# Kernel tuning notes

Measured on AMD Instinct MI355X. Metric: run time of the kernel, lower is better.

The kernel has to match this reference:

```python
import jax, jax.numpy as jnp
import numpy as np

B, S, D = 4, 4096, 1024
STATE = 1024
HID = 4 * D
EPS_NORM = 1e-6           # RMSNorm module eps
EPS_FP32 = 1.1920929e-7   # torch F.rms_norm default eps = finfo(fp32).eps


def rms_norm(x, eps):
    # no learned weight (RMSNorm(dim=-1) has weight=None)
    return x * jax.lax.rsqrt(jnp.mean(jnp.square(x), axis=-1, keepdims=True) + eps)


def setup_inputs() -> dict:
    key = jax.random.key(0)
    ks = jax.random.split(key, 8)
    scale_d = 1.0 / np.sqrt(D)
    scale_s = 1.0 / np.sqrt(STATE)
    scale_h = 1.0 / np.sqrt(HID)
    return {
        "x": jax.random.normal(ks[0], (B, S, D), jnp.float32),
        "x0": jax.random.normal(ks[1], (B, S, D), jnp.float32),
        "Wu": jax.random.normal(ks[2], (STATE, D), jnp.float32) * scale_d,
        "Wg": jax.random.normal(ks[3], (STATE, D), jnp.float32) * scale_d,
        "Wo": jax.random.normal(ks[4], (D, STATE), jnp.float32) * scale_s,
        "Wfc": jax.random.normal(ks[5], (HID, D), jnp.float32) * scale_d,
        "Wproj": jax.random.normal(ks[6], (D, HID), jnp.float32) * scale_h,
        "memory_mix": jnp.ones((D,), jnp.float32),
        "mlp_scale": jnp.ones((D,), jnp.float32),
        "resid_mix": jnp.stack([jnp.ones((D,), jnp.float32), jnp.zeros((D,), jnp.float32)]),
    }


def reference(x, x0, Wu, Wg, Wo, Wfc, Wproj, memory_mix, mlp_scale, resid_mix):
    # residual mix of x and x0
    x = resid_mix[0][None, None, :] * x + resid_mix[1][None, None, :] * x0

    # --- CausalPrefixMemory branch ---
    h = rms_norm(x, EPS_NORM)
    update = jnp.einsum('bsd,kd->bsk', h, Wu)
    gate = jax.nn.sigmoid(jnp.einsum('bsd,kd->bsk', h, Wg))
    memory = jnp.cumsum(gate * update, axis=1)          # [B,S,STATE]
    denom = jnp.arange(1, S + 1, dtype=jnp.float32)[None, :, None]
    m = rms_norm(memory / denom, EPS_FP32)
    mem_out = jnp.einsum('bsk,dk->bsd', m, Wo)
    x = x + memory_mix[None, None, :] * mem_out

    # --- MLP branch: relu^2 ---
    h2 = rms_norm(x, EPS_NORM)
    r = jax.nn.relu(jnp.einsum('bsd,hd->bsh', h2, Wfc))
    mlp_out = jnp.einsum('bsh,dh->bsd', jnp.square(r), Wproj)
    x = x + mlp_scale[None, None, :] * mlp_out
    return x
```

## Files before the change

kernel.cpp:

```cpp
#include <hip/hip_runtime.h>
#include <stdint.h>

typedef unsigned short u16;
typedef __attribute__((ext_vector_type(8))) short s16x8;
typedef __attribute__((ext_vector_type(4))) float f32x4;

__device__ __forceinline__ u16 f2bf(float f) {
  uint32_t u = __float_as_uint(f);
  uint32_t r = (u + 0x7FFFu + ((u >> 16) & 1u)) >> 16;
  return (u16)r;
}

__device__ __forceinline__ void gll16(const void* g, void* lds) {
  __builtin_amdgcn_global_load_lds(
      (const __attribute__((address_space(1))) uint32_t*)g,
      (__attribute__((address_space(3))) uint32_t*)lds, 16, 0, 0);
}

__device__ __forceinline__ void xcd_swz(int& bx, int& by) {
  int gx = gridDim.x;
  int lin = blockIdx.y * gx + blockIdx.x;
  int cpx = (gx * gridDim.y) >> 3;
  int nl = (lin & 7) * cpx + (lin >> 3);
  bx = nl % gx;
  by = nl / gx;
}

__global__ __launch_bounds__(256) void k_f2b(const float* __restrict__ src,
                                             u16* __restrict__ dst, int n) {
  int i = (blockIdx.x * 256 + threadIdx.x) * 4;
  if (i < n) {
    float4 v = *(const float4*)(src + i);
    ushort4 o;
    o.x = f2bf(v.x); o.y = f2bf(v.y); o.z = f2bf(v.z); o.w = f2bf(v.w);
    *(ushort4*)(dst + i) = o;
  }
}

template <bool MIX>
__global__ __launch_bounds__(256) void k_rms(const float* __restrict__ X,
                                             const float* __restrict__ X0,
                                             const float* __restrict__ rmix,
                                             float* __restrict__ XMout,
                                             u16* __restrict__ Hout, float eps) {
  const int row = blockIdx.x, t = threadIdx.x;
  const size_t base = (size_t)row * 1024;
  float4 v;
  if (MIX) {
    float4 a = ((const float4*)(X + base))[t];
    float4 b = ((const float4*)(X0 + base))[t];
    float4 c0 = ((const float4*)rmix)[t];
    float4 c1 = ((const float4*)(rmix + 1024))[t];
    v.x = c0.x * a.x + c1.x * b.x;
    v.y = c0.y * a.y + c1.y * b.y;
    v.z = c0.z * a.z + c1.z * b.z;
    v.w = c0.w * a.w + c1.w * b.w;
  } else {
    v = ((const float4*)(X + base))[t];
  }
  float ss = v.x * v.x + v.y * v.y + v.z * v.z + v.w * v.w;
#pragma unroll
  for (int o = 32; o > 0; o >>= 1) ss += __shfl_xor(ss, o);
  __shared__ float red[4];
  if ((t & 63) == 0) red[t >> 6] = ss;
  __syncthreads();
  float tot = red[0] + red[1] + red[2] + red[3];
  float sc = rsqrtf(tot * (1.0f / 1024.0f) + eps);
  if (MIX) ((float4*)(XMout + base))[t] = v;
  ushort4 hv;
  hv.x = f2bf(v.x * sc); hv.y = f2bf(v.y * sc);
  hv.z = f2bf(v.z * sc); hv.w = f2bf(v.w * sc);
  ((ushort4*)(Hout + base))[t] = hv;
}

__global__ __launch_bounds__(256) void k_scan1(const float* __restrict__ P,
                                               float* __restrict__ CS) {
  int blk = blockIdx.x;
  int chunk = blk & 255, b = blk >> 8;
  const float4* p = (const float4*)(P + ((size_t)b * 4096 + chunk * 16) * 1024)
                    + threadIdx.x;
  float4 s = {0.f, 0.f, 0.f, 0.f};
#pragma unroll
  for (int i = 0; i < 16; ++i) {
    float4 v = p[(size_t)i * 256];
    s.x += v.x; s.y += v.y; s.z += v.z; s.w += v.w;
  }
  ((float4*)(CS + ((size_t)b * 256 + chunk) * 1024))[threadIdx.x] = s;
}

__global__ __launch_bounds__(256) void k_scan2(float* __restrict__ CS) {
  int idx = blockIdx.x * 256 + threadIdx.x;
  int b = idx >> 10, k = idx & 1023;
  float run = 0.f;
  for (int c = 0; c < 256; ++c) {
    size_t o = ((size_t)b * 256 + c) * 1024 + k;
    float v = CS[o];
    CS[o] = run;
    run += v;
  }
}

__global__ __launch_bounds__(64) void k_scan3f(const float* __restrict__ P,
                                               const float* __restrict__ CS,
                                               u16* __restrict__ Mout) {
  int blk = blockIdx.x;
  int chunk = blk & 255, b = blk >> 8;
  const int t = threadIdx.x;
  const float4* cs4 = (const float4*)(CS + ((size_t)b * 256 + chunk) * 1024);
  float4 run[4];
#pragma unroll
  for (int q = 0; q < 4; ++q) run[q] = cs4[q * 64 + t];
  const float4* p4 = (const float4*)(P + ((size_t)b * 4096 + chunk * 16) * 1024);
  u16* mo = Mout + ((size_t)b * 4096 + chunk * 16) * 1024;
  const int rowbase = chunk * 16;
#pragma unroll 2
  for (int i = 0; i < 16; ++i) {
    float4 v[4];
#pragma unroll
    for (int q = 0; q < 4; ++q) v[q] = p4[(size_t)i * 256 + q * 64 + t];
    const float inv = 1.0f / (float)(rowbase + i + 1);
    float4 y[4];
    float ss = 0.f;
#pragma unroll
    for (int q = 0; q < 4; ++q) {
      run[q].x += v[q].x; run[q].y += v[q].y;
      run[q].z += v[q].z; run[q].w += v[q].w;
      y[q].x = run[q].x * inv; y[q].y = run[q].y * inv;
      y[q].z = run[q].z * inv; y[q].w = run[q].w * inv;
      ss += y[q].x * y[q].x + y[q].y * y[q].y
          + y[q].z * y[q].z + y[q].w * y[q].w;
    }
#pragma unroll
    for (int o = 32; o > 0; o >>= 1) ss += __shfl_xor(ss, o);
    float sc = rsqrtf(ss * (1.0f / 1024.0f) + 1.1920929e-7f);
#pragma unroll
    for (int q = 0; q < 4; ++q) {
      ushort4 hv;
      hv.x = f2bf(y[q].x * sc); hv.y = f2bf(y[q].y * sc);
      hv.z = f2bf(y[q].z * sc); hv.w = f2bf(y[q].w * sc);
      *(ushort4*)(mo + (size_t)i * 1024 + (q * 64 + t) * 4) = hv;
    }
  }
}

__global__ __launch_bounds__(256, 2) void gemm_dual(
    const u16* __restrict__ A, const u16* __restrict__ Bu,
    const u16* __restrict__ Bg, float* __restrict__ P, int K) {
  __shared__ __align__(16) u16 As[128 * 64];
  __shared__ __align__(16) u16 Us[64 * 64];
  __shared__ __align__(16) u16 Gs[64 * 64];
  const int t = threadIdx.x;
  const int lane = t & 63, wid = t >> 6;
  int bx, by;
  xcd_swz(bx, by);
  const int m0 = by * 128, n0 = bx * 64;
  const int wm = wid * 32;
  const int l15 = lane & 15, lhi = lane >> 4;

  size_t gA[4], gU[2];
#pragma unroll
  for (int i = 0; i < 4; ++i) {
    int j = i * 256 + t;
    int row = j >> 3;
    int k16 = (j & 7) ^ (row & 7);
    gA[i] = (size_t)(m0 + row) * K + k16 * 8;
  }
#pragma unroll
  for (int i = 0; i < 2; ++i) {
    int j = i * 256 + t;
    int row = j >> 3;
    int k16 = (j & 7) ^ (row & 7);
    gU[i] = (size_t)(n0 + row) * K + k16 * 8;
  }

  f32x4 au[2][4], ag[2][4];
#pragma unroll
  for (int mi = 0; mi < 2; ++mi)
#pragma unroll
    for (int ni = 0; ni < 4; ++ni) { au[mi][ni] = 0.0f; ag[mi][ni] = 0.0f; }

  for (int kb = 0; kb < K; kb += 64) {
#pragma unroll
    for (int i = 0; i < 4; ++i) {
      int j = i * 256 + t;
      gll16(A + gA[i] + kb, &As[j * 8]);
    }
#pragma unroll
    for (int i = 0; i < 2; ++i) {
      int j = i * 256 + t;
      gll16(Bu + gU[i] + kb, &Us[j * 8]);
      gll16(Bg + gU[i] + kb, &Gs[j * 8]);
    }
    __syncthreads();
#pragma unroll
    for (int kc = 0; kc < 2; ++kc) {
      s16x8 af[2], uf[4], gf[4];
#pragma unroll
      for (int mi = 0; mi < 2; ++mi) {
        int row = wm + mi * 16 + l15;
        int k16 = (kc * 4 + lhi) ^ (row & 7);
        af[mi] = *(const s16x8*)&As[row * 64 + k16 * 8];
      }
#pragma unroll
      for (int ni = 0; ni < 4; ++ni) {
        int row = ni * 16 + l15;
        int k16 = (kc * 4 + lhi) ^ (row & 7);
        uf[ni] = *(const s16x8*)&Us[row * 64 + k16 * 8];
        gf[ni] = *(const s16x8*)&Gs[row * 64 + k16 * 8];
      }
#pragma unroll
      for (int mi = 0; mi < 2; ++mi)
#pragma unroll
        for (int ni = 0; ni < 4; ++ni) {
          au[mi][ni] = __builtin_amdgcn_mfma_f32_16x16x32_bf16(
              af[mi], uf[ni], au[mi][ni], 0, 0, 0);
          ag[mi][ni] = __builtin_amdgcn_mfma_f32_16x16x32_bf16(
              af[mi], gf[ni], ag[mi][ni], 0, 0, 0);
        }
    }
    __syncthreads();
  }

#pragma unroll
  for (int mi = 0; mi < 2; ++mi) {
    int r0 = m0 + wm + mi * 16 + lhi * 4;
#pragma unroll
    for (int ni = 0; ni < 4; ++ni) {
      int c = n0 + ni * 16 + l15;
#pragma unroll
      for (int j = 0; j < 4; ++j) {
        float u = au[mi][ni][j], g = ag[mi][ni][j];
        P[(size_t)(r0 + j) * 1024 + c] = u / (1.0f + __expf(-g));
      }
    }
  }
}

template <int EPI>
__global__ __launch_bounds__(256, 2) void gemm_bf16(
    const u16* __restrict__ A, const u16* __restrict__ Bw, void* __restrict__ Cout,
    const float* __restrict__ Cadd, const float* __restrict__ colscale,
    int K, int lda, int ldb, int ldc) {
  __shared__ __align__(16) u16 As[128 * 64];
  __shared__ __align__(16) u16 Bs[128 * 64];
  const int t = threadIdx.x;
  const int lane = t & 63, wid = t >> 6;
  int bx, by;
  xcd_swz(bx, by);
  const int m0 = by * 128, n0 = bx * 128;
  const int wm = (wid >> 1) * 64, wn = (wid & 1) * 64;
  const int l15 = lane & 15, lhi = lane >> 4;

  size_t gA[4], gB[4];
#pragma unroll
  for (int i = 0; i < 4; ++i) {
    int j = i * 256 + t;
    int row = j >> 3;
    int k16 = (j & 7) ^ (row & 7);
    gA[i] = (size_t)(m0 + row) * lda + k16 * 8;
    gB[i] = (size_t)(n0 + row) * ldb + k16 * 8;
  }

  f32x4 acc[4][4];
#pragma unroll
  for (int mi = 0; mi < 4; ++mi)
#pragma unroll
    for (int ni = 0; ni < 4; ++ni) acc[mi][ni] = 0.0f;

  for (int kb = 0; kb < K; kb += 64) {
#pragma unroll
    for (int i = 0; i < 4; ++i) {
      int j = i * 256 + t;
      gll16(A + gA[i] + kb, &As[j * 8]);
      gll16(Bw + gB[i] + kb, &Bs[j * 8]);
    }
    __syncthreads();
#pragma unroll
    for (int kc = 0; kc < 2; ++kc) {
      s16x8 af[4], bfr[4];
#pragma unroll
      for (int mi = 0; mi < 4; ++mi) {
        int row = wm + mi * 16 + l15;
        int k16 = (kc * 4 + lhi) ^ (row & 7);
        af[mi] = *(const s16x8*)&As[row * 64 + k16 * 8];
      }
#pragma unroll
      for (int ni = 0; ni < 4; ++ni) {
        int row = wn + ni * 16 + l15;
        int k16 = (kc * 4 + lhi) ^ (row & 7);
        bfr[ni] = *(const s16x8*)&Bs[row * 64 + k16 * 8];
      }
#pragma unroll
      for (int mi = 0; mi < 4; ++mi)
#pragma unroll
        for (int ni = 0; ni < 4; ++ni)
          acc[mi][ni] = __builtin_amdgcn_mfma_f32_16x16x32_bf16(
              af[mi], bfr[ni], acc[mi][ni], 0, 0, 0);
    }
    __syncthreads();
  }

#pragma unroll
  for (int mi = 0; mi < 4; ++mi) {
    int r0 = m0 + wm + mi * 16 + lhi * 4;
#pragma unroll
    for (int ni = 0; ni < 4; ++ni) {
      int c = n0 + wn + ni * 16 + l15;
      float cs = (EPI == 1) ? colscale[c] : 0.f;
#pragma unroll
      for (int j = 0; j < 4; ++j) {
        size_t idx = (size_t)(r0 + j) * ldc + c;
        float v = acc[mi][ni][j];
        if (EPI == 1) {
          ((float*)Cout)[idx] = Cadd[idx] + cs * v;
        } else {
          float rv = fmaxf(v, 0.f);
          ((u16*)Cout)[idx] = f2bf(rv * rv);
        }
      }
    }
  }
}

extern "C" void kernel_launch(void* const* d_in, const int* in_sizes, int n_in,
                              void* d_out, int out_size, void* d_ws, size_t ws_size,
                              hipStream_t stream) {
  const float* x = (const float*)d_in[0];
  const float* x0 = (const float*)d_in[1];
  const float* Wu = (const float*)d_in[2];
  const float* Wg = (const float*)d_in[3];
  const float* Wo = (const float*)d_in[4];
  const float* Wfc = (const float*)d_in[5];
  const float* Wpj = (const float*)d_in[6];
  const float* mmix = (const float*)d_in[7];
  const float* mscale = (const float*)d_in[8];
  const float* rmix = (const float*)d_in[9];
  float* out = (float*)d_out;

  const int M = 16384;
  const size_t MiB = 1024 * 1024;

  char* ws = (char*)d_ws;
  u16* WuB = (u16*)ws;   ws += 2 * MiB;
  u16* WgB = (u16*)ws;   ws += 2 * MiB;
  u16* WoB = (u16*)ws;   ws += 2 * MiB;
  u16* WfcB = (u16*)ws;  ws += 8 * MiB;
  u16* WpjB = (u16*)ws;  ws += 8 * MiB;
  u16* h = (u16*)ws;     ws += 32 * MiB;
  char* pool = ws;
  float* P = (float*)pool;
  float* CS = (float*)(pool + 64 * MiB);
  u16* mB = (u16*)(pool + 68 * MiB);
  u16* R2 = (u16*)pool;
  float* xm = out;

  const bool fullR2 = ws_size >= 182 * MiB;

  k_f2b<<<1024, 256, 0, stream>>>(Wu, WuB, 1024 * 1024);
  k_f2b<<<1024, 256, 0, stream>>>(Wg, WgB, 1024 * 1024);
  k_f2b<<<1024, 256, 0, stream>>>(Wo, WoB, 1024 * 1024);
  k_f2b<<<4096, 256, 0, stream>>>(Wfc, WfcB, 4096 * 1024);
  k_f2b<<<4096, 256, 0, stream>>>(Wpj, WpjB, 4096 * 1024);

  k_rms<true><<<M, 256, 0, stream>>>(x, x0, rmix, xm, h, 1e-6f);

  gemm_dual<<<dim3(16, 128), 256, 0, stream>>>(h, WuB, WgB, P, 1024);

  k_scan1<<<1024, 256, 0, stream>>>(P, CS);
  k_scan2<<<16, 256, 0, stream>>>(CS);
  k_scan3f<<<1024, 64, 0, stream>>>(P, CS, mB);

  gemm_bf16<1><<<dim3(8, 128), 256, 0, stream>>>(mB, WoB, xm, xm, mmix,
                                                 1024, 1024, 1024, 1024);
  k_rms<false><<<M, 256, 0, stream>>>(xm, nullptr, nullptr, nullptr, h, 1e-6f);

  if (fullR2) {
    gemm_bf16<2><<<dim3(32, 128), 256, 0, stream>>>(
        h, WfcB, R2, nullptr, nullptr, 1024, 1024, 1024, 4096);
    gemm_bf16<1><<<dim3(8, 128), 256, 0, stream>>>(
        R2, WpjB, out, out, mscale, 4096, 4096, 4096, 1024);
  } else {
    for (int c = 0; c < 2; ++c) {
      gemm_bf16<2><<<dim3(16, 128), 256, 0, stream>>>(
          h, WfcB + (size_t)c * 2048 * 1024, R2, nullptr, nullptr,
          1024, 1024, 1024, 2048);
      gemm_bf16<1><<<dim3(8, 128), 256, 0, stream>>>(
          R2, WpjB + (size_t)c * 2048, out, out, mscale,
          2048, 2048, 4096, 1024);
    }
  }
}
```

Measured before the change: 520.3 us.

## Replace 128x128 GEMM with 256x256 eight-wave double-buffered pipelined kernel

Replaces the simple single-buffered 128x128 bf16 GEMM with a 256x256-tile, 512-thread kernel. It double-buffers LDS and interleaves next-tile global_load_lds issues with MFMA phases, using explicit barriers, waitcnt and setprio. The aim is to hide global-load latency and raise arithmetic intensity per block for the Wo, Wfc and Wproj GEMMs. The cost is 128KB of LDS and one block per CU, which gives fewer blocks and possible wave-quantization at the smaller grid sizes. Hand-tuned vmcnt counts also raise correctness risk.

Result: slower. 548.1 us (+5.3%).

```diff
diff --git a/kernel.cpp b/kernel.cpp
--- a/kernel.cpp
+++ b/kernel.cpp
@@ -236,76 +236,137 @@
   }
 }
 
+#define SA8(SQ, HF, KB)                                                      \
+  { _Pragma("unroll") for (int c = 0; c < 2; ++c)                            \
+      gll16(A + aoff[c] + (size_t)(HF) * 128 * lda + (KB),                   \
+            (u16*)As + ((SQ) * 2 + (HF)) * 8192 + lo[c]); }
+#define SB8(SQ, HF, KB)                                                      \
+  { _Pragma("unroll") for (int c = 0; c < 2; ++c)                            \
+      gll16(Bw + boff[c] + (size_t)(HF) * 128 * ldb + (KB),                  \
+            (u16*)Bs + ((SQ) * 2 + (HF)) * 8192 + lo[c]); }
+
+#define PH8(PAR, KC, MH, CHK0, STGSTMT, VMSTMT)                              \
+  {                                                                          \
+    if (CHK0) {                                                              \
+      STGSTMT;                                                               \
+      VMSTMT;                                                                \
+      __builtin_amdgcn_s_barrier();                                          \
+      __builtin_amdgcn_sched_barrier(0);                                     \
+    }                                                                        \
+    s16x8 af[4];                                                             \
+    _Pragma("unroll") for (int j = 0; j < 4; ++j) {                          \
+      int row = ((MH) * 4 + j) * 16 + l15;                                   \
+      int cph = (((KC) * 4 + lhi) ^ (row & 7));                              \
+      af[j] = *(const s16x8*)((const u16*)As + ((PAR) * 2 + wr) * 8192       \
+                              + row * 64 + cph * 8);                         \
+    }                                                                        \
+    if ((MH) == 0) {                                                         \
+      _Pragma("unroll") for (int ni = 0; ni < 4; ++ni) {                     \
+        int row = rb + ni * 16 + l15;                                        \
+        int cph = (((KC) * 4 + lhi) ^ (row & 7));                            \
+        bf[ni] = *(const s16x8*)((const u16*)Bs + ((PAR) * 2 + hb) * 8192    \
+                                 + row * 64 + cph * 8);                      \
+      }                                                                      \
+    }                                                                        \
+    if (!(CHK0)) {                                                           \
+      STGSTMT;                                                               \
+      __builtin_amdgcn_s_barrier();                                          \
+    }                                                                        \
+    asm volatile("s_waitcnt lgkmcnt(0)" ::: "memory");                       \
+    __builtin_amdgcn_sched_barrier(0);                                       \
+    __builtin_amdgcn_s_setprio(1);                                           \
+    _Pragma("unroll") for (int j = 0; j < 4; ++j)                            \
+      _Pragma("unroll") for (int ni = 0; ni < 4; ++ni)                       \
+        acc[(MH) * 4 + j][ni] = __builtin_amdgcn_mfma_f32_16x16x32_bf16(     \
+            af[j], bf[ni], acc[(MH) * 4 + j][ni], 0, 0, 0);                  \
+    __builtin_amdgcn_s_setprio(0);                                           \
+    __builtin_amdgcn_s_barrier();                                            \
+    __builtin_amdgcn_sched_barrier(0);                                       \
+  }
+
 template <int EPI>
-__global__ __launch_bounds__(256, 2) void gemm_bf16(
-    const u16* __restrict__ A, const u16* __restrict__ Bw, void* __restrict__ Cout,
-    const float* __restrict__ Cadd, const float* __restrict__ colscale,
-    int K, int lda, int ldb, int ldc) {
-  __shared__ __align__(16) u16 As[128 * 64];
-  __shared__ __align__(16) u16 Bs[128 * 64];
+__global__ __launch_bounds__(512, 1) void gemm8p(
+    const u16* __restrict__ A, const u16* __restrict__ Bw,
+    void* __restrict__ Cout, const float* __restrict__ Cadd,
+    const float* __restrict__ colscale, int K, int lda, int ldb, int ldc) {
+  __shared__ __align__(16) u16 As[2][2][128][64];
+  __shared__ __align__(16) u16 Bs[2][2][128][64];
   const int t = threadIdx.x;
   const int lane = t & 63, wid = t >> 6;
   int bx, by;
   xcd_swz(bx, by);
-  const int m0 = by * 128, n0 = bx * 128;
-  const int wm = (wid >> 1) * 64, wn = (wid & 1) * 64;
+  const int m0 = by * 256, n0 = bx * 256;
+  const int wr = wid >> 2, wc = wid & 3;
   const int l15 = lane & 15, lhi = lane >> 4;
-
-  size_t gA[4], gB[4];
-#pragma unroll
-  for (int i = 0; i < 4; ++i) {
-    int j = i * 256 + t;
-    int row = j >> 3;
-    int k16 = (j & 7) ^ (row & 7);
-    gA[i] = (size_t)(m0 + row) * lda + k16 * 8;
-    gB[i] = (size_t)(n0 + row) * ldb + k16 * 8;
-  }
-
-  f32x4 acc[4][4];
-#pragma unroll
-  for (int mi = 0; mi < 4; ++mi)
+  const int hb = wc >> 1;
+  const int rb = (wc & 1) * 64;
+
+  uint32_t aoff[2], boff[2];
+  int lo[2];
+#pragma unroll
+  for (int c = 0; c < 2; ++c) {
+    int j = c * 512 + t;
+    int row = j >> 3, p8 = j & 7;
+    int lg = p8 ^ (row & 7);
+    aoff[c] = (uint32_t)(m0 + row) * lda + lg * 8;
+    boff[c] = (uint32_t)(n0 + row) * ldb + lg * 8;
+    lo[c] = j * 8;
+  }
+
+  f32x4 acc[8][4];
+#pragma unroll
+  for (int mi = 0; mi < 8; ++mi)
 #pragma unroll
     for (int ni = 0; ni < 4; ++ni) acc[mi][ni] = 0.0f;
 
-  for (int kb = 0; kb < K; kb += 64) {
-#pragma unroll
-    for (int i = 0; i < 4; ++i) {
-      int j = i * 256 + t;
-      gll16(A + gA[i] + kb, &As[j * 8]);
-      gll16(Bw + gB[i] + kb, &Bs[j * 8]);
-    }
-    __syncthreads();
-#pragma unroll
-    for (int kc = 0; kc < 2; ++kc) {
-      s16x8 af[4], bfr[4];
-#pragma unroll
-      for (int mi = 0; mi < 4; ++mi) {
-        int row = wm + mi * 16 + l15;
-        int k16 = (kc * 4 + lhi) ^ (row & 7);
-        af[mi] = *(const s16x8*)&As[row * 64 + k16 * 8];
+  const int nt = K >> 6;
+
+#pragma unroll
+  for (int kt = 0; kt < 2; ++kt)
+#pragma unroll
+    for (int hf = 0; hf < 2; ++hf)
+#pragma unroll
+      for (int c = 0; c < 2; ++c) {
+        gll16(A + aoff[c] + (size_t)hf * 128 * lda + kt * 64,
+              (u16*)As + (kt * 2 + hf) * 8192 + lo[c]);
+        gll16(Bw + boff[c] + (size_t)hf * 128 * ldb + kt * 64,
+              (u16*)Bs + (kt * 2 + hf) * 8192 + lo[c]);
       }
-#pragma unroll
-      for (int ni = 0; ni < 4; ++ni) {
-        int row = wn + ni * 16 + l15;
-        int k16 = (kc * 4 + lhi) ^ (row & 7);
-        bfr[ni] = *(const s16x8*)&Bs[row * 64 + k16 * 8];
-      }
-#pragma unroll
-      for (int mi = 0; mi < 4; ++mi)
-#pragma unroll
-        for (int ni = 0; ni < 4; ++ni)
-          acc[mi][ni] = __builtin_amdgcn_mfma_f32_16x16x32_bf16(
-              af[mi], bfr[ni], acc[mi][ni], 0, 0, 0);
-    }
-    __syncthreads();
-  }
-
-#pragma unroll
-  for (int mi = 0; mi < 4; ++mi) {
-    int r0 = m0 + wm + mi * 16 + lhi * 4;
+  asm volatile("s_waitcnt vmcnt(8)" ::: "memory");
+  __builtin_amdgcn_s_barrier();
+  __builtin_amdgcn_sched_barrier(0);
+
+  s16x8 bf[4];
+
+  PH8(0, 0, 0, true, , )
+  PH8(0, 0, 1, false, , )
+  PH8(0, 1, 0, false, , )
+  PH8(0, 1, 1, false, , )
+
+  for (int kt = 1; kt < nt - 1; ++kt) {
+    const int par = kt & 1, sq = par ^ 1;
+    const uint32_t kb = (uint32_t)(kt + 1) * 64;
+    PH8(par, 0, 0, true, SA8(sq, 0, kb),
+        asm volatile("s_waitcnt vmcnt(2)" ::: "memory"))
+    PH8(par, 0, 1, false, SB8(sq, 0, kb), )
+    PH8(par, 1, 0, false, SA8(sq, 1, kb), )
+    PH8(par, 1, 1, false, SB8(sq, 1, kb), )
+  }
+
+  {
+    const int par = (nt - 1) & 1;
+    PH8(par, 0, 0, true, , asm volatile("s_waitcnt vmcnt(0)" ::: "memory"))
+    PH8(par, 0, 1, false, , )
+    PH8(par, 1, 0, false, , )
+    PH8(par, 1, 1, false, , )
+  }
+
+#pragma unroll
+  for (int mi = 0; mi < 8; ++mi) {
+    int r0 = m0 + wr * 128 + mi * 16 + lhi * 4;
 #pragma unroll
     for (int ni = 0; ni < 4; ++ni) {
-      int c = n0 + wn + ni * 16 + l15;
+      int c = n0 + wc * 64 + ni * 16 + l15;
       float cs = (EPI == 1) ? colscale[c] : 0.f;
 #pragma unroll
       for (int j = 0; j < 4; ++j) {
@@ -370,21 +431,21 @@
   k_scan2<<<16, 256, 0, stream>>>(CS);
   k_scan3f<<<1024, 64, 0, stream>>>(P, CS, mB);
 
-  gemm_bf16<1><<<dim3(8, 128), 256, 0, stream>>>(mB, WoB, xm, xm, mmix,
-                                                 1024, 1024, 1024, 1024);
+  gemm8p<1><<<dim3(4, 64), 512, 0, stream>>>(mB, WoB, xm, xm, mmix,
+                                             1024, 1024, 1024, 1024);
   k_rms<false><<<M, 256, 0, stream>>>(xm, nullptr, nullptr, nullptr, h, 1e-6f);
 
   if (fullR2) {
-    gemm_bf16<2><<<dim3(32, 128), 256, 0, stream>>>(
+    gemm8p<2><<<dim3(16, 64), 512, 0, stream>>>(
         h, WfcB, R2, nullptr, nullptr, 1024, 1024, 1024, 4096);
-    gemm_bf16<1><<<dim3(8, 128), 256, 0, stream>>>(
+    gemm8p<1><<<dim3(4, 64), 512, 0, stream>>>(
         R2, WpjB, out, out, mscale, 4096, 4096, 4096, 1024);
   } else {
     for (int c = 0; c < 2; ++c) {
-      gemm_bf16<2><<<dim3(16, 128), 256, 0, stream>>>(
+      gemm8p<2><<<dim3(8, 64), 512, 0, stream>>>(
           h, WfcB + (size_t)c * 2048 * 1024, R2, nullptr, nullptr,
           1024, 1024, 1024, 2048);
-      gemm_bf16<1><<<dim3(8, 128), 256, 0, stream>>>(
+      gemm8p<1><<<dim3(4, 64), 512, 0, stream>>>(
           R2, WpjB + (size_t)c * 2048, out, out, mscale,
           2048, 2048, 4096, 1024);
     }
```
